# Performance work log

Measured on AMD Instinct MI355X. Metric: run time of the kernel, lower is better.

## Reference

```python
import jax, jax.numpy as jnp
import numpy as np
from jax import lax

N_Q = 4          # kernel_size**2 for Q_conv(kernel_size=2)
DIM = 16         # 2**N_Q statevector dimension
N_LAYERS = 3

# --- static circuit constants -------------------------------------------

def _cnot_np(c, t):
    # PennyLane convention: wire 0 is the most-significant bit.
    M = np.zeros((DIM, DIM), np.complex64)
    for s in range(DIM):
        s2 = s ^ (1 << (N_Q - 1 - t)) if (s >> (N_Q - 1 - c)) & 1 else s
        M[s2, s] = 1.0
    return jnp.asarray(M)

# StronglyEntanglingLayers: layer l uses range r = l % (n_wires-1) + 1
_CNOTS = {r: [_cnot_np(i, (i + r) % N_Q) for i in range(N_Q)] for r in (1, 2, 3)}

_ZDIAG = jnp.asarray(np.array(
    [[1.0 - 2.0 * ((s >> (N_Q - 1 - w)) & 1) for w in range(N_Q)] for s in range(DIM)],
    np.float32))  # (16, 4): diag of PauliZ on each wire


def _rot(p):
    # qml.Rot(phi, theta, omega) = RZ(omega) RY(theta) RZ(phi)
    phi, th, om = p[0], p[1], p[2]
    c, s = jnp.cos(th / 2), jnp.sin(th / 2)
    r0 = jnp.stack([jnp.exp(-1j * (phi + om) / 2) * c, -jnp.exp(1j * (phi - om) / 2) * s])
    r1 = jnp.stack([jnp.exp(-1j * (phi - om) / 2) * s, jnp.exp(1j * (phi + om) / 2) * c])
    return jnp.stack([r0, r1]).astype(jnp.complex64)


def _circuit_unitary(qw):
    # qw: (3, 4, 3). One StronglyEntanglingLayers block of 3 layers,
    # which the qnode applies n_layers=3 times with the SAME weights.
    U = jnp.eye(DIM, dtype=jnp.complex64)
    for l in range(N_LAYERS):
        L = _rot(qw[l, 0])
        for q in range(1, N_Q):
            L = jnp.kron(L, _rot(qw[l, q]))
        for C in _CNOTS[l + 1]:
            L = C @ L
        U = L @ U
    return U @ U @ U


def _quanv(x, qw):
    # x: (B, 1, 44, 44); k = stride = 2 -> non-overlapping 2x2 patches.
    B, H = x.shape[0], x.shape[-1]
    o = H // 2  # 22
    patches = x.reshape(B, o, 2, o, 2).transpose(0, 1, 3, 2, 4).reshape(-1, 4)
    # AngleEmbedding (RX) on |0000> gives a product state.
    a = jnp.cos(patches / 2).astype(jnp.complex64)
    b = (-1j * jnp.sin(patches / 2)).astype(jnp.complex64)
    w = jnp.stack([a, b], axis=-1)  # (N, 4, 2)
    psi0 = jnp.einsum('na,nb,nc,nd->nabcd', w[:, 0], w[:, 1], w[:, 2], w[:, 3]).reshape(-1, DIM)
    psi = psi0 @ _circuit_unitary(qw).T  # (N, 16)
    probs = psi.real ** 2 + psi.imag ** 2
    e = probs @ _ZDIAG  # (N, 4) expvals of PauliZ per wire
    return e.reshape(B, o * o, N_Q).transpose(0, 2, 1).reshape(B, N_Q, o, o).astype(x.dtype)


def _conv(x, w, b, stride):
    y = lax.conv_general_dilated(x, w, (stride, stride), 'VALID',
                                 dimension_numbers=('NCHW', 'OIHW', 'NCHW'))
    return y + b[None, :, None, None]


def _maxpool(x, k, s):
    return lax.reduce_window(x, -jnp.inf, lax.max, (1, 1, k, k), (1, 1, s, s), 'VALID')


def setup_inputs() -> dict:
    key = jax.random.key(0)
    ks = jax.random.split(key, 18)
    B = 256
    f32 = jnp.float32
    return {
        'x': jax.random.normal(ks[0], (B, 1, 186, 186), f32),
        'conv1_w': jax.random.normal(ks[1], (1, 1, 8, 8), f32) * 0.1,
        'conv1_b': jax.random.normal(ks[2], (1,), f32) * 0.05,
        'q_w': jax.random.uniform(ks[3], (3, 4, 3), f32, 0.0, 2.0 * np.pi),
        'conv2_w': jax.random.normal(ks[4], (32, 4, 4, 4), f32) * 0.1,
        'conv2_b': jax.random.normal(ks[5], (32,), f32) * 0.05,
        'conv3_w': jax.random.normal(ks[6], (64, 32, 4, 4), f32) * 0.05,
        'conv3_b': jax.random.normal(ks[7], (64,), f32) * 0.05,
        'conv4_w': jax.random.normal(ks[8], (128, 64, 4, 4), f32) * 0.03,
        'conv4_b': jax.random.normal(ks[9], (128,), f32) * 0.05,
        'fc1_w': jax.random.normal(ks[10], (128, 3200), f32) * 0.02,
        'fc1_b': jax.random.normal(ks[11], (128,), f32) * 0.05,
        'fc2_w': jax.random.normal(ks[12], (64, 128), f32) * 0.09,
        'fc2_b': jax.random.normal(ks[13], (64,), f32) * 0.05,
        'fc3_w': jax.random.normal(ks[14], (16, 64), f32) * 0.12,
        'fc3_b': jax.random.normal(ks[15], (16,), f32) * 0.05,
        'fc4_w': jax.random.normal(ks[16], (2, 16), f32) * 0.25,
        'fc4_b': jax.random.normal(ks[17], (2,), f32) * 0.05,
    }


def reference(x, conv1_w, conv1_b, q_w, conv2_w, conv2_b, conv3_w, conv3_b,
              conv4_w, conv4_b, fc1_w, fc1_b, fc2_w, fc2_b, fc3_w, fc3_b,
              fc4_w, fc4_b):
    h = _maxpool(jnp.tanh(_conv(x, conv1_w, conv1_b, 2)), 4, 2) * (np.pi / 2)
    h = jax.nn.relu(_quanv(h, q_w))                       # (B, 4, 22, 22)
    h = _maxpool(jax.nn.relu(_conv(h, conv2_w, conv2_b, 1)), 4, 1)
    h = _maxpool(jax.nn.relu(_conv(h, conv3_w, conv3_b, 1)), 2, 1)
    h = jax.nn.relu(_conv(h, conv4_w, conv4_b, 2))        # (B, 128, 5, 5)
    h = h.reshape(h.shape[0], -1)
    h = jax.nn.relu(h @ fc1_w.T + fc1_b)   # dropout: eval mode = identity
    h = jax.nn.relu(h @ fc2_w.T + fc2_b)
    h = jax.nn.relu(h @ fc3_w.T + fc3_b)
    return jax.nn.log_softmax(h @ fc4_w.T + fc4_b, axis=1)
```

## Files before the change

### kernel.cpp

```cpp
#include <hip/hip_runtime.h>
#include <hip/hip_bf16.h>
#include <math.h>


__device__ __forceinline__ float2 cmul(float2 a, float2 b) {
    return make_float2(a.x * b.x - a.y * b.y, a.x * b.y + a.y * b.x);
}
__device__ __forceinline__ float2 cfma(float2 a, float2 b, float2 acc) {
    acc.x += a.x * b.x - a.y * b.y;
    acc.y += a.x * b.y + a.y * b.x;
    return acc;
}

__global__ __launch_bounds__(256) void k_build_V(const float* __restrict__ qw,
                                                 float2* __restrict__ Vout) {
    __shared__ float2 rot[3][4][2][2];
    __shared__ float2 L[16][16];
    __shared__ float2 U[16][16];
    __shared__ float2 T[16][16];

    int tid = threadIdx.x;
    if (tid < 12) {
        int l = tid >> 2, q = tid & 3;
        float phi = qw[(l * 4 + q) * 3 + 0];
        float th  = qw[(l * 4 + q) * 3 + 1];
        float om  = qw[(l * 4 + q) * 3 + 2];
        float c, s;
        sincosf(0.5f * th, &s, &c);
        float sa, ca, sb, cb;
        sincosf(0.5f * (phi + om), &sa, &ca);
        sincosf(0.5f * (phi - om), &sb, &cb);
        rot[l][q][0][0] = make_float2( ca * c, -sa * c);
        rot[l][q][0][1] = make_float2(-cb * s, -sb * s);
        rot[l][q][1][0] = make_float2( cb * s, -sb * s);
        rot[l][q][1][1] = make_float2( ca * c,  sa * c);
    }
    int s = tid >> 4, t = tid & 15;
    U[s][t] = make_float2((s == t) ? 1.f : 0.f, 0.f);
    __syncthreads();

    for (int l = 0; l < 3; ++l) {
        int r = l + 1;
        int ss = s;
        for (int i = 3; i >= 0; --i) {
            int c_ = i, t_ = (i + r) & 3;
            if ((ss >> (3 - c_)) & 1) ss ^= 1 << (3 - t_);
        }
        float2 v = make_float2(1.f, 0.f);
        #pragma unroll
        for (int q = 0; q < 4; ++q) {
            int bs = (ss >> (3 - q)) & 1;
            int bt = (t  >> (3 - q)) & 1;
            v = cmul(v, rot[l][q][bs][bt]);
        }
        L[s][t] = v;
        __syncthreads();
        float2 acc = make_float2(0.f, 0.f);
        #pragma unroll
        for (int k = 0; k < 16; ++k) acc = cfma(L[s][k], U[k][t], acc);
        T[s][t] = acc;
        __syncthreads();
        U[s][t] = T[s][t];
        __syncthreads();
    }
    float2 acc = make_float2(0.f, 0.f);
    #pragma unroll
    for (int k = 0; k < 16; ++k) acc = cfma(U[s][k], U[k][t], acc);
    T[s][t] = acc;
    __syncthreads();
    acc = make_float2(0.f, 0.f);
    #pragma unroll
    for (int k = 0; k < 16; ++k) acc = cfma(T[s][k], U[k][t], acc);
    int pc = __popc(t) & 3;
    float2 v;
    if      (pc == 0) v = acc;
    else if (pc == 1) v = make_float2( acc.y, -acc.x);
    else if (pc == 2) v = make_float2(-acc.x, -acc.y);
    else              v = make_float2(-acc.y,  acc.x);
    Vout[s * 16 + t] = v;
}

__global__ __launch_bounds__(256) void k_wtrans(const float* __restrict__ w3,
                                                const float* __restrict__ w4,
                                                float* __restrict__ wt3,
                                                float* __restrict__ wt4) {
    int idx = blockIdx.x * 256 + threadIdx.x;
    if (idx < 32768) {
        int oc = idx & 63, tap = (idx >> 6) & 15, ic = idx >> 10;
        wt3[idx] = w3[oc * 512 + ic * 16 + tap];
    } else {
        int o = idx - 32768;
        int oc = o & 127, tap = (o >> 7) & 15, ic = o >> 11;
        wt4[o] = w4[oc * 1024 + ic * 16 + tap];
    }
}

__global__ __launch_bounds__(256) void k_conv1d(const float* __restrict__ x,
                                                const float* __restrict__ w,
                                                const float* __restrict__ bias,
                                                float* __restrict__ y) {
    int idx = blockIdx.x * 256 + threadIdx.x;
    int j = idx % 90;
    int t = idx / 90;
    int i = t % 90;
    int b = t / 90;
    const float* xb = x + b * 34596 + (2 * i) * 186 + 2 * j;
    float acc = bias[0];
    #pragma unroll
    for (int u = 0; u < 8; ++u) {
        const float* rp = xb + u * 186;
        float2 p0 = *(const float2*)(rp + 0);
        float2 p1 = *(const float2*)(rp + 2);
        float2 p2 = *(const float2*)(rp + 4);
        float2 p3 = *(const float2*)(rp + 6);
        acc = fmaf(w[u * 8 + 0], p0.x, acc);
        acc = fmaf(w[u * 8 + 1], p0.y, acc);
        acc = fmaf(w[u * 8 + 2], p1.x, acc);
        acc = fmaf(w[u * 8 + 3], p1.y, acc);
        acc = fmaf(w[u * 8 + 4], p2.x, acc);
        acc = fmaf(w[u * 8 + 5], p2.y, acc);
        acc = fmaf(w[u * 8 + 6], p3.x, acc);
        acc = fmaf(w[u * 8 + 7], p3.y, acc);
    }
    y[idx] = tanhf(acc);
}

__global__ __launch_bounds__(256) void k_quanvp(const float* __restrict__ y,
                                                const float2* __restrict__ Vg,
                                                float* __restrict__ o) {
    __shared__ float2 V[256];
    V[threadIdx.x] = Vg[threadIdx.x];
    __syncthreads();

    int idx = blockIdx.x * 256 + threadIdx.x;
    int j = idx % 22;
    int t = idx / 22;
    int i = t % 22;
    int b = t / 22;

    const float* yb = y + b * 8100 + (4 * i) * 90 + 4 * j;
    float ra[6], rb[6];
    #pragma unroll
    for (int r = 0; r < 6; ++r) {
        const float* rp = yb + r * 90;
        float2 p0 = *(const float2*)(rp);
        float2 p1 = *(const float2*)(rp + 2);
        float2 p2 = *(const float2*)(rp + 4);
        float m01 = fmaxf(p0.x, p0.y);
        float m23 = fmaxf(p1.x, p1.y);
        float m45 = fmaxf(p2.x, p2.y);
        ra[r] = fmaxf(m01, m23);
        rb[r] = fmaxf(m23, m45);
    }
    const float S = 1.57079632679489662f;
    float a0 = S * fmaxf(fmaxf(ra[0], ra[1]), fmaxf(ra[2], ra[3]));
    float a1 = S * fmaxf(fmaxf(rb[0], rb[1]), fmaxf(rb[2], rb[3]));
    float a2 = S * fmaxf(fmaxf(ra[2], ra[3]), fmaxf(ra[4], ra[5]));
    float a3 = S * fmaxf(fmaxf(rb[2], rb[3]), fmaxf(rb[4], rb[5]));

    float cs[4], sn[4];
    sincosf(0.5f * a0, &sn[0], &cs[0]);
    sincosf(0.5f * a1, &sn[1], &cs[1]);
    sincosf(0.5f * a2, &sn[2], &cs[2]);
    sincosf(0.5f * a3, &sn[3], &cs[3]);

    float c[16];
    #pragma unroll
    for (int tt = 0; tt < 16; ++tt) {
        c[tt] = ((tt & 8) ? sn[0] : cs[0]) * ((tt & 4) ? sn[1] : cs[1]) *
                ((tt & 2) ? sn[2] : cs[2]) * ((tt & 1) ? sn[3] : cs[3]);
    }

    float e0 = 0.f, e1 = 0.f, e2 = 0.f, e3 = 0.f;
    #pragma unroll
    for (int s = 0; s < 16; ++s) {
        float re = 0.f, im = 0.f;
        #pragma unroll
        for (int tt = 0; tt < 16; ++tt) {
            float2 v = V[s * 16 + tt];
            re = fmaf(v.x, c[tt], re);
            im = fmaf(v.y, c[tt], im);
        }
        float pr = re * re + im * im;
        e0 += (s & 8) ? -pr : pr;
        e1 += (s & 4) ? -pr : pr;
        e2 += (s & 2) ? -pr : pr;
        e3 += (s & 1) ? -pr : pr;
    }
    float* ob = o + b * (4 * 484) + i * 22 + j;
    ob[0]    = fmaxf(e0, 0.f);
    ob[484]  = fmaxf(e1, 0.f);
    ob[968]  = fmaxf(e2, 0.f);
    ob[1452] = fmaxf(e3, 0.f);
}

__global__ __launch_bounds__(640) void k_conv2t(const float* __restrict__ x,
                                                const float* __restrict__ w,
                                                const float* __restrict__ bias,
                                                float* __restrict__ y) {
    __shared__ float Xs[4 * 22 * 28];
    __shared__ float Ws[32 * 68];
    int b = blockIdx.x;
    int tid = threadIdx.x;

    const float* xb = x + b * 1936;
    for (int k = tid; k < 1936; k += 640) {
        int ic = k / 484, rem = k % 484;
        int r = rem / 22, c = rem % 22;
        Xs[ic * 616 + r * 28 + c] = xb[k];
    }
    for (int k = tid; k < 2048; k += 640) {
        Ws[(k >> 6) * 68 + (k & 63)] = w[k];
    }
    __syncthreads();

    if (tid < 608) {
        int oc = tid / 19, i = tid % 19;
        float acc[19];
        float bv = bias[oc];
        #pragma unroll
        for (int j = 0; j < 19; ++j) acc[j] = bv;
        const float* wr = &Ws[oc * 68];
        #pragma unroll
        for (int ic = 0; ic < 4; ++ic) {
            #pragma unroll
            for (int u = 0; u < 4; ++u) {
                const float* rp = &Xs[ic * 616 + (i + u) * 28];
                float xr[22];
                #pragma unroll
                for (int k = 0; k < 5; ++k)
                    *(float4*)&xr[4 * k] = *(const float4*)(rp + 4 * k);
                *(float2*)&xr[20] = *(const float2*)(rp + 20);
                float4 wv = *(const float4*)(wr + ic * 16 + u * 4);
                #pragma unroll
                for (int j = 0; j < 19; ++j) {
                    acc[j] = fmaf(wv.x, xr[j],     acc[j]);
                    acc[j] = fmaf(wv.y, xr[j + 1], acc[j]);
                    acc[j] = fmaf(wv.z, xr[j + 2], acc[j]);
                    acc[j] = fmaf(wv.w, xr[j + 3], acc[j]);
                }
            }
        }
        float* yp = y + b * 11552 + oc * 361 + i * 19;
        #pragma unroll
        for (int j = 0; j < 19; ++j) yp[j] = fmaxf(acc[j], 0.f);
    }
}

__global__ __launch_bounds__(256) void k_pool2(const float* __restrict__ x,
                                               float* __restrict__ y) {
    int idx = blockIdx.x * 256 + threadIdx.x;
    int j = idx % 16;
    int t = idx / 16;
    int i = t % 16;
    int c = t / 16;
    const float* xb = x + c * 361 + i * 19 + j;
    float m = -INFINITY;
    #pragma unroll
    for (int u = 0; u < 4; ++u)
        #pragma unroll
        for (int v = 0; v < 4; ++v)
            m = fmaxf(m, xb[u * 19 + v]);
    y[idx] = m;
}

__global__ __launch_bounds__(448) void k_conv3x(const float* __restrict__ x,
                                                const float* __restrict__ wt3,
                                                const float* __restrict__ bias,
                                                float* __restrict__ y) {
    __shared__ float Xs[32 * 200];
    __shared__ float Rs[224 * 26];
    int bid = blockIdx.x;
    int b = bid >> 1, h = bid & 1;
    int r0 = h * 7;
    int nr = 7 - h;
    int tid = threadIdx.x;

    const float* xb = x + b * 8192 + r0 * 16;
    #pragma unroll
    for (int it = 0; it < 3; ++it) {
        int k = it * 448 + tid;
        if (k < 1280) {
            int ic = k / 40, rem = k % 40;
            int r = rem >> 2, c4 = rem & 3;
            if (r0 + r < 16) {
                float4 v = *(const float4*)(xb + ic * 256 + r * 16 + c4 * 4);
                *(float4*)(&Xs[ic * 200 + r * 20 + c4 * 4]) = v;
            }
        }
    }
    __syncthreads();

    int kg = (tid >= 224) ? 1 : 0;
    int t2 = tid - kg * 224;
    int ocp = t2 & 31, il = t2 >> 5;
    int oc0 = ocp * 2;

    float acc0[13], acc1[13];
    #pragma unroll
    for (int j = 0; j < 13; ++j) { acc0[j] = 0.f; acc1[j] = 0.f; }

    const float* wb = wt3 + kg * 16384 + oc0;
    for (int k = 0; k < 16; ++k) {
        const float* wp = wb + k * 1024;
        float2 cw[16];
        #pragma unroll
        for (int t = 0; t < 16; ++t) cw[t] = *(const float2*)(wp + t * 64);

        const float* xc = &Xs[(kg * 16 + k) * 200 + il * 20];
        #pragma unroll
        for (int u = 0; u < 4; ++u) {
            float xr[16];
            const float* rp = xc + u * 20;
            #pragma unroll
            for (int kk = 0; kk < 4; ++kk)
                *(float4*)&xr[4 * kk] = *(const float4*)(rp + 4 * kk);
            #pragma unroll
            for (int j = 0; j < 13; ++j) {
                #pragma unroll
                for (int v = 0; v < 4; ++v) {
                    acc0[j] = fmaf(cw[u * 4 + v].x, xr[j + v], acc0[j]);
                    acc1[j] = fmaf(cw[u * 4 + v].y, xr[j + v], acc1[j]);
                }
            }
        }
    }

    if (kg == 1) {
        float* rp = &Rs[t2 * 26];
        #pragma unroll
        for (int j = 0; j < 13; ++j) { rp[j] = acc0[j]; rp[13 + j] = acc1[j]; }
    }
    __syncthreads();

    if (kg == 0 && il < nr) {
        const float* rp = &Rs[t2 * 26];
        float bv0 = bias[oc0], bv1 = bias[oc0 + 1];
        float* yp = y + b * 10816 + oc0 * 169 + (r0 + il) * 13;
        #pragma unroll
        for (int j = 0; j < 13; ++j) {
            yp[j]       = fmaxf(acc0[j] + rp[j]      + bv0, 0.f);
            yp[169 + j] = fmaxf(acc1[j] + rp[13 + j] + bv1, 0.f);
        }
    }
}

__global__ __launch_bounds__(640) void k_conv4s(const float* __restrict__ x3,
                                                const float* __restrict__ wt4,
                                                float* __restrict__ part) {
    __shared__ float Xs[32 * 144];
    __shared__ float Rs[320 * 10];
    int bid = blockIdx.x;
    int b = bid >> 1, kq = bid & 1;
    int tid = threadIdx.x;

    const float* gb = x3 + b * 10816 + kq * 32 * 169;
    for (int k = tid; k < 4608; k += 640) {
        int ic = k / 144, rc = k % 144;
        int r = rc / 12, c = rc % 12;
        const float* g = gb + ic * 169 + r * 13 + c;
        float m = fmaxf(fmaxf(g[0], g[1]), fmaxf(g[13], g[14]));
        Xs[k] = m;
    }
    __syncthreads();

    int kg = (tid >= 320) ? 1 : 0;
    int t2 = tid - kg * 320;
    int ocp = t2 & 63, i = t2 >> 6;
    int oc0 = ocp * 2;

    float acc0[5], acc1[5];
    #pragma unroll
    for (int j = 0; j < 5; ++j) { acc0[j] = 0.f; acc1[j] = 0.f; }

    const float* wb = wt4 + kq * 65536 + kg * 32768 + oc0;
    for (int k = 0; k < 16; ++k) {
        const float* wp = wb + k * 2048;
        float2 cw[16];
        #pragma unroll
        for (int t = 0; t < 16; ++t) cw[t] = *(const float2*)(wp + t * 128);

        const float* xc = &Xs[(kg * 16 + k) * 144];
        #pragma unroll
        for (int u = 0; u < 4; ++u) {
            const float* rp = xc + (2 * i + u) * 12;
            float xr[12];
            #pragma unroll
            for (int kk = 0; kk < 3; ++kk)
                *(float4*)&xr[4 * kk] = *(const float4*)(rp + 4 * kk);
            #pragma unroll
            for (int j = 0; j < 5; ++j) {
                #pragma unroll
                for (int v = 0; v < 4; ++v) {
                    acc0[j] = fmaf(cw[u * 4 + v].x, xr[2 * j + v], acc0[j]);
                    acc1[j] = fmaf(cw[u * 4 + v].y, xr[2 * j + v], acc1[j]);
                }
            }
        }
    }

    if (kg == 1) {
        float* rp = &Rs[t2 * 10];
        #pragma unroll
        for (int j = 0; j < 5; ++j) { rp[j] = acc0[j]; rp[5 + j] = acc1[j]; }
    }
    __syncthreads();

    if (kg == 0) {
        const float* rp = &Rs[t2 * 10];
        float* pp = part + kq * 819200 + b * 3200 + oc0 * 25 + i * 5;
        #pragma unroll
        for (int j = 0; j < 5; ++j) {
            pp[j]      = acc0[j] + rp[j];
            pp[25 + j] = acc1[j] + rp[5 + j];
        }
    }
}

__global__ __launch_bounds__(256) void k_c4red(const float* __restrict__ part,
                                               const float* __restrict__ bias,
                                               float* __restrict__ y) {
    int idx = blockIdx.x * 256 + threadIdx.x;
    float s = part[idx] + part[idx + 819200];
    int oc = (idx / 25) & 127;
    y[idx] = fmaxf(s + bias[oc], 0.f);
}

__global__ __launch_bounds__(256) void k_fc1t(const float* __restrict__ x,
                                              const float* __restrict__ w,
                                              const float* __restrict__ bias,
                                              float* __restrict__ y) {
    __shared__ float Ls[4][32][65];
    int bid = blockIdx.x;
    int ig = bid >> 2, ocg = bid & 3;
    int imgB = ig * 4, ocB = ocg * 32;
    int tid = threadIdx.x, lane = tid & 63, wv = tid >> 6;
    int ocW = ocB + wv * 8;

    float acc[8][4];
    #pragma unroll
    for (int o = 0; o < 8; ++o)
        #pragma unroll
        for (int m = 0; m < 4; ++m) acc[o][m] = 0.f;

    for (int it = 0; it < 25; ++it) {
        int k = it * 128 + lane * 2;
        float2 xv[4];
        #pragma unroll
        for (int m = 0; m < 4; ++m)
            xv[m] = *(const float2*)&x[(imgB + m) * 3200 + k];
        #pragma unroll
        for (int o = 0; o < 8; ++o) {
            float2 wvv = *(const float2*)&w[(ocW + o) * 3200 + k];
            #pragma unroll
            for (int m = 0; m < 4; ++m) {
                acc[o][m] = fmaf(wvv.x, xv[m].x, acc[o][m]);
                acc[o][m] = fmaf(wvv.y, xv[m].y, acc[o][m]);
            }
        }
    }
    #pragma unroll
    for (int o = 0; o < 8; ++o)
        #pragma unroll
        for (int m = 0; m < 4; ++m)
            Ls[wv][o * 4 + m][lane] = acc[o][m];
    __syncthreads();

    if (tid < 128) {
        int w2 = tid >> 5, r = tid & 31;
        const float* p = Ls[w2][r];
        float s = 0.f;
        #pragma unroll
        for (int c = 0; c < 64; ++c) s += p[c];
        int o = r >> 2, m = r & 3;
        int oc = ocB + w2 * 8 + o;
        y[(imgB + m) * 128 + oc] = fmaxf(s + bias[oc], 0.f);
    }
}

__global__ __launch_bounds__(64) void k_fc_tail(const float* __restrict__ x,
                                                const float* __restrict__ w2,
                                                const float* __restrict__ b2,
                                                const float* __restrict__ w3,
                                                const float* __restrict__ b3,
                                                const float* __restrict__ w4,
                                                const float* __restrict__ b4,
                                                float* __restrict__ out) {
    __shared__ float xs[128], h2[64], h3[16];
    int img = blockIdx.x;
    int lane = threadIdx.x;

    *(float2*)&xs[lane * 2] = *(const float2*)&x[img * 128 + lane * 2];
    __syncthreads();

    float a = b2[lane];
    const float4* wp = (const float4*)&w2[lane * 128];
    const float4* xp = (const float4*)xs;
    #pragma unroll
    for (int k = 0; k < 32; ++k) {
        float4 wv = wp[k], xv = xp[k];
        a = fmaf(wv.x, xv.x, a);
        a = fmaf(wv.y, xv.y, a);
        a = fmaf(wv.z, xv.z, a);
        a = fmaf(wv.w, xv.w, a);
    }
    h2[lane] = fmaxf(a, 0.f);
    __syncthreads();

    if (lane < 16) {
        float a3 = b3[lane];
        const float4* w3p = (const float4*)&w3[lane * 64];
        const float4* h2p = (const float4*)h2;
        #pragma unroll
        for (int k = 0; k < 16; ++k) {
            float4 wv = w3p[k], xv = h2p[k];
            a3 = fmaf(wv.x, xv.x, a3);
            a3 = fmaf(wv.y, xv.y, a3);
            a3 = fmaf(wv.z, xv.z, a3);
            a3 = fmaf(wv.w, xv.w, a3);
        }
        h3[lane] = fmaxf(a3, 0.f);
    }
    __syncthreads();

    if (lane == 0) {
        float z0 = b4[0], z1 = b4[1];
        #pragma unroll
        for (int k = 0; k < 16; ++k) {
            z0 = fmaf(w4[k],      h3[k], z0);
            z1 = fmaf(w4[16 + k], h3[k], z1);
        }
        float m = fmaxf(z0, z1);
        float lse = m + logf(expf(z0 - m) + expf(z1 - m));
        out[img * 2 + 0] = z0 - lse;
        out[img * 2 + 1] = z1 - lse;
    }
}

extern "C" void kernel_launch(void* const* d_in, const int* in_sizes, int n_in,
                              void* d_out, int out_size, void* d_ws, size_t ws_size,
                              hipStream_t stream) {
    const float* x       = (const float*)d_in[0];
    const float* conv1_w = (const float*)d_in[1];
    const float* conv1_b = (const float*)d_in[2];
    const float* q_w     = (const float*)d_in[3];
    const float* conv2_w = (const float*)d_in[4];
    const float* conv2_b = (const float*)d_in[5];
    const float* conv3_w = (const float*)d_in[6];
    const float* conv3_b = (const float*)d_in[7];
    const float* conv4_w = (const float*)d_in[8];
    const float* conv4_b = (const float*)d_in[9];
    const float* fc1_w   = (const float*)d_in[10];
    const float* fc1_b   = (const float*)d_in[11];
    const float* fc2_w   = (const float*)d_in[12];
    const float* fc2_b   = (const float*)d_in[13];
    const float* fc3_w   = (const float*)d_in[14];
    const float* fc3_b   = (const float*)d_in[15];
    const float* fc4_w   = (const float*)d_in[16];
    const float* fc4_b   = (const float*)d_in[17];
    float* out = (float*)d_out;

    char* ws = (char*)d_ws;
    float2* V  = (float2*)ws;
    float* A   = (float*)(ws + 4096);
    float* B   = (float*)(ws + 12587008);
    float* WT3 = (float*)(ws + 21499904);
    float* WT4 = (float*)(ws + 21639168);

    k_build_V<<<1, 256, 0, stream>>>(q_w, V);
    k_wtrans<<<640, 256, 0, stream>>>(conv3_w, conv4_w, WT3, WT4);
    k_conv1d<<<8100, 256, 0, stream>>>(x, conv1_w, conv1_b, A);
    k_quanvp<<<484, 256, 0, stream>>>(A, V, B);
    k_conv2t<<<256, 640, 0, stream>>>(B, conv2_w, conv2_b, A);
    k_pool2<<<8192, 256, 0, stream>>>(A, B);
    k_conv3x<<<512, 448, 0, stream>>>(B, WT3, conv3_b, A);
    k_conv4s<<<512, 640, 0, stream>>>(A, WT4, B);
    k_c4red<<<3200, 256, 0, stream>>>(B, conv4_b, A);
    k_fc1t<<<256, 256, 0, stream>>>(A, fc1_w, fc1_b, B);
    k_fc_tail<<<256, 64, 0, stream>>>(B, fc2_w, fc2_b, fc3_w, fc3_b,
                                      fc4_w, fc4_b, out);
}
```

Measured before the change: 176.2 us.

## Register-block 4 output channels per thread in conv3/conv4, split input channels four ways

The conv3 and conv4 kernels now compute 4 output channels per thread instead of 2 and split the input-channel reduction across 4 thread groups instead of 2. Weights are read as float4 inside the loop rather than preloaded into 16 registers. Partial sums are combined through shared memory in three sequential synchronized steps. This raises FMA work per input load and cuts the per-thread loop length, at the cost of more accumulator registers and extra barriers in the reduction.

```diff
diff --git a/kernel.cpp b/kernel.cpp
--- a/kernel.cpp
+++ b/kernel.cpp
@@ -264,12 +264,12 @@
     y[idx] = m;
 }
 
-__global__ __launch_bounds__(448) void k_conv3x(const float* __restrict__ x,
+__global__ __launch_bounds__(448) void k_conv3y(const float* __restrict__ x,
                                                 const float* __restrict__ wt3,
                                                 const float* __restrict__ bias,
                                                 float* __restrict__ y) {
     __shared__ float Xs[32 * 200];
-    __shared__ float Rs[224 * 26];
+    __shared__ float Rs[112 * 56];
     int bid = blockIdx.x;
     int b = bid >> 1, h = bid & 1;
     int r0 = h * 7;
@@ -291,23 +291,21 @@
     }
     __syncthreads();
 
-    int kg = (tid >= 224) ? 1 : 0;
-    int t2 = tid - kg * 224;
-    int ocp = t2 & 31, il = t2 >> 5;
-    int oc0 = ocp * 2;
-
-    float acc0[13], acc1[13];
-    #pragma unroll
-    for (int j = 0; j < 13; ++j) { acc0[j] = 0.f; acc1[j] = 0.f; }
-
-    const float* wb = wt3 + kg * 16384 + oc0;
-    for (int k = 0; k < 16; ++k) {
+    int kg = tid / 112;
+    int t2 = tid - kg * 112;
+    int ocq = t2 & 15, il = t2 >> 4;
+    int oc0 = ocq * 4;
+
+    float acc[4][13];
+    #pragma unroll
+    for (int o = 0; o < 4; ++o)
+        #pragma unroll
+        for (int j = 0; j < 13; ++j) acc[o][j] = 0.f;
+
+    const float* wb = wt3 + kg * 8192 + oc0;
+    for (int k = 0; k < 8; ++k) {
         const float* wp = wb + k * 1024;
-        float2 cw[16];
-        #pragma unroll
-        for (int t = 0; t < 16; ++t) cw[t] = *(const float2*)(wp + t * 64);
-
-        const float* xc = &Xs[(kg * 16 + k) * 200 + il * 20];
+        const float* xc = &Xs[(kg * 8 + k) * 200 + il * 20];
         #pragma unroll
         for (int u = 0; u < 4; ++u) {
             float xr[16];
@@ -316,40 +314,60 @@
             for (int kk = 0; kk < 4; ++kk)
                 *(float4*)&xr[4 * kk] = *(const float4*)(rp + 4 * kk);
             #pragma unroll
-            for (int j = 0; j < 13; ++j) {
+            for (int v = 0; v < 4; ++v) {
+                float4 wv = *(const float4*)(wp + (u * 4 + v) * 64);
                 #pragma unroll
-                for (int v = 0; v < 4; ++v) {
-                    acc0[j] = fmaf(cw[u * 4 + v].x, xr[j + v], acc0[j]);
-                    acc1[j] = fmaf(cw[u * 4 + v].y, xr[j + v], acc1[j]);
+                for (int j = 0; j < 13; ++j) {
+                    acc[0][j] = fmaf(wv.x, xr[j + v], acc[0][j]);
+                    acc[1][j] = fmaf(wv.y, xr[j + v], acc[1][j]);
+                    acc[2][j] = fmaf(wv.z, xr[j + v], acc[2][j]);
+                    acc[3][j] = fmaf(wv.w, xr[j + v], acc[3][j]);
                 }
             }
         }
     }
 
-    if (kg == 1) {
-        float* rp = &Rs[t2 * 26];
-        #pragma unroll
-        for (int j = 0; j < 13; ++j) { rp[j] = acc0[j]; rp[13 + j] = acc1[j]; }
-    }
-    __syncthreads();
+    #pragma unroll
+    for (int g = 1; g < 4; ++g) {
+        __syncthreads();
+        if (kg == g) {
+            float* rp = &Rs[t2 * 56];
+            #pragma unroll
+            for (int o = 0; o < 4; ++o) {
+                *(float4*)(rp + o * 13 + 0) = make_float4(acc[o][0], acc[o][1], acc[o][2], acc[o][3]);
+                *(float4*)(rp + o * 13 + 4) = make_float4(acc[o][4], acc[o][5], acc[o][6], acc[o][7]);
+                *(float4*)(rp + o * 13 + 8) = make_float4(acc[o][8], acc[o][9], acc[o][10], acc[o][11]);
+                rp[o * 13 + 12] = acc[o][12];
+            }
+        }
+        __syncthreads();
+        if (kg == 0) {
+            const float* rp = &Rs[t2 * 56];
+            #pragma unroll
+            for (int o = 0; o < 4; ++o)
+                #pragma unroll
+                for (int j = 0; j < 13; ++j)
+                    acc[o][j] += rp[o * 13 + j];
+        }
+    }
 
     if (kg == 0 && il < nr) {
-        const float* rp = &Rs[t2 * 26];
-        float bv0 = bias[oc0], bv1 = bias[oc0 + 1];
         float* yp = y + b * 10816 + oc0 * 169 + (r0 + il) * 13;
         #pragma unroll
-        for (int j = 0; j < 13; ++j) {
-            yp[j]       = fmaxf(acc0[j] + rp[j]      + bv0, 0.f);
-            yp[169 + j] = fmaxf(acc1[j] + rp[13 + j] + bv1, 0.f);
-        }
-    }
-}
-
-__global__ __launch_bounds__(640) void k_conv4s(const float* __restrict__ x3,
+        for (int o = 0; o < 4; ++o) {
+            float bv = bias[oc0 + o];
+            #pragma unroll
+            for (int j = 0; j < 13; ++j)
+                yp[o * 169 + j] = fmaxf(acc[o][j] + bv, 0.f);
+        }
+    }
+}
+
+__global__ __launch_bounds__(640) void k_conv4y(const float* __restrict__ x3,
                                                 const float* __restrict__ wt4,
                                                 float* __restrict__ part) {
     __shared__ float Xs[32 * 144];
-    __shared__ float Rs[320 * 10];
+    __shared__ float Rs[160 * 24];
     int bid = blockIdx.x;
     int b = bid >> 1, kq = bid & 1;
     int tid = threadIdx.x;
@@ -364,23 +382,21 @@
     }
     __syncthreads();
 
-    int kg = (tid >= 320) ? 1 : 0;
-    int t2 = tid - kg * 320;
-    int ocp = t2 & 63, i = t2 >> 6;
-    int oc0 = ocp * 2;
-
-    float acc0[5], acc1[5];
-    #pragma unroll
-    for (int j = 0; j < 5; ++j) { acc0[j] = 0.f; acc1[j] = 0.f; }
-
-    const float* wb = wt4 + kq * 65536 + kg * 32768 + oc0;
-    for (int k = 0; k < 16; ++k) {
+    int kg = tid / 160;
+    int t2 = tid - kg * 160;
+    int ocq = t2 & 31, i = t2 >> 5;
+    int oc0 = ocq * 4;
+
+    float acc[4][5];
+    #pragma unroll
+    for (int o = 0; o < 4; ++o)
+        #pragma unroll
+        for (int j = 0; j < 5; ++j) acc[o][j] = 0.f;
+
+    const float* wb = wt4 + (kq * 32 + kg * 8) * 2048 + oc0;
+    for (int k = 0; k < 8; ++k) {
         const float* wp = wb + k * 2048;
-        float2 cw[16];
-        #pragma unroll
-        for (int t = 0; t < 16; ++t) cw[t] = *(const float2*)(wp + t * 128);
-
-        const float* xc = &Xs[(kg * 16 + k) * 144];
+        const float* xc = &Xs[(kg * 8 + k) * 144];
         #pragma unroll
         for (int u = 0; u < 4; ++u) {
             const float* rp = xc + (2 * i + u) * 12;
@@ -389,31 +405,45 @@
             for (int kk = 0; kk < 3; ++kk)
                 *(float4*)&xr[4 * kk] = *(const float4*)(rp + 4 * kk);
             #pragma unroll
-            for (int j = 0; j < 5; ++j) {
+            for (int v = 0; v < 4; ++v) {
+                float4 wv = *(const float4*)(wp + (u * 4 + v) * 128);
                 #pragma unroll
-                for (int v = 0; v < 4; ++v) {
-                    acc0[j] = fmaf(cw[u * 4 + v].x, xr[2 * j + v], acc0[j]);
-                    acc1[j] = fmaf(cw[u * 4 + v].y, xr[2 * j + v], acc1[j]);
+                for (int j = 0; j < 5; ++j) {
+                    acc[0][j] = fmaf(wv.x, xr[2 * j + v], acc[0][j]);
+                    acc[1][j] = fmaf(wv.y, xr[2 * j + v], acc[1][j]);
+                    acc[2][j] = fmaf(wv.z, xr[2 * j + v], acc[2][j]);
+                    acc[3][j] = fmaf(wv.w, xr[2 * j + v], acc[3][j]);
                 }
             }
         }
     }
 
-    if (kg == 1) {
-        float* rp = &Rs[t2 * 10];
-        #pragma unroll
-        for (int j = 0; j < 5; ++j) { rp[j] = acc0[j]; rp[5 + j] = acc1[j]; }
-    }
-    __syncthreads();
+    #pragma unroll
+    for (int g = 1; g < 4; ++g) {
+        __syncthreads();
+        if (kg == g) {
+            float* rp = &Rs[t2 * 24];
+            #pragma unroll
+            for (int o = 0; o < 4; ++o)
+                #pragma unroll
+                for (int j = 0; j < 5; ++j) rp[o * 5 + j] = acc[o][j];
+        }
+        __syncthreads();
+        if (kg == 0) {
+            const float* rp = &Rs[t2 * 24];
+            #pragma unroll
+            for (int o = 0; o < 4; ++o)
+                #pragma unroll
+                for (int j = 0; j < 5; ++j) acc[o][j] += rp[o * 5 + j];
+        }
+    }
 
     if (kg == 0) {
-        const float* rp = &Rs[t2 * 10];
         float* pp = part + kq * 819200 + b * 3200 + oc0 * 25 + i * 5;
         #pragma unroll
-        for (int j = 0; j < 5; ++j) {
-            pp[j]      = acc0[j] + rp[j];
-            pp[25 + j] = acc1[j] + rp[5 + j];
-        }
+        for (int o = 0; o < 4; ++o)
+            #pragma unroll
+            for (int j = 0; j < 5; ++j) pp[o * 25 + j] = acc[o][j];
     }
 }
 
@@ -573,8 +603,8 @@
     k_quanvp<<<484, 256, 0, stream>>>(A, V, B);
     k_conv2t<<<256, 640, 0, stream>>>(B, conv2_w, conv2_b, A);
     k_pool2<<<8192, 256, 0, stream>>>(A, B);
-    k_conv3x<<<512, 448, 0, stream>>>(B, WT3, conv3_b, A);
-    k_conv4s<<<512, 640, 0, stream>>>(A, WT4, B);
+    k_conv3y<<<512, 448, 0, stream>>>(B, WT3, conv3_b, A);
+    k_conv4y<<<512, 640, 0, stream>>>(A, WT4, B);
     k_c4red<<<3200, 256, 0, stream>>>(B, conv4_b, A);
     k_fc1t<<<256, 256, 0, stream>>>(A, fc1_w, fc1_b, B);
     k_fc_tail<<<256, 64, 0, stream>>>(B, fc2_w, fc2_b, fc3_w, fc3_b,
```

Result: faster. 164.2 us (-6.8%).
